# Kernel optimization log

Hardware: AMD Instinct MI355X
Metric: run time of the kernel (lower is better)

The kernel has to match this reference:

```python
import jax, jax.numpy as jnp
import numpy as np

NUM_SLOTS = 8
DIM = 256
ITERS = 3
EPS_LN = 1e-5

def _ln(x, g, b):
    mu = jnp.mean(x, axis=-1, keepdims=True)
    var = jnp.var(x, axis=-1, keepdims=True)
    return (x - mu) * jax.lax.rsqrt(var + EPS_LN) * g + b

def setup_inputs() -> dict:
    key = jax.random.key(0)
    ks = jax.random.split(key, 16)
    d = DIM
    s = 1.0 / np.sqrt(d)
    inp = {
        'x': jax.random.normal(ks[0], (64, 4096, d), jnp.float32),
        'noise': jax.random.normal(ks[1], (64, NUM_SLOTS, d), jnp.float32),
        'slots_mu': jax.random.normal(ks[2], (1, 1, d), jnp.float32),
        'slots_logsigma': jnp.zeros((1, 1, d), jnp.float32),
        'Wq': jax.random.uniform(ks[3], (d, d), jnp.float32, -s, s),
        'Wk': jax.random.uniform(ks[4], (d, d), jnp.float32, -s, s),
        'Wv': jax.random.uniform(ks[5], (d, d), jnp.float32, -s, s),
        'W_ih': jax.random.uniform(ks[6], (3 * d, d), jnp.float32, -s, s),
        'W_hh': jax.random.uniform(ks[7], (3 * d, d), jnp.float32, -s, s),
        'b_ih': jax.random.uniform(ks[8], (3 * d,), jnp.float32, -s, s),
        'b_hh': jax.random.uniform(ks[9], (3 * d,), jnp.float32, -s, s),
        'W1': jax.random.uniform(ks[10], (d, d), jnp.float32, -s, s),
        'b1': jax.random.uniform(ks[11], (d,), jnp.float32, -s, s),
        'W2': jax.random.uniform(ks[12], (d, d), jnp.float32, -s, s),
        'b2': jax.random.uniform(ks[13], (d,), jnp.float32, -s, s),
        'g_in': jnp.ones((d,), jnp.float32), 'be_in': jnp.zeros((d,), jnp.float32),
        'g_sl': jnp.ones((d,), jnp.float32), 'be_sl': jnp.zeros((d,), jnp.float32),
        'g_ff': jnp.ones((d,), jnp.float32), 'be_ff': jnp.zeros((d,), jnp.float32),
    }
    return inp

def _gru(x, h, W_ih, W_hh, b_ih, b_hh):
    # torch.nn.GRUCell math; x,h: [M, d]
    gi = x @ W_ih.T + b_ih
    gh = h @ W_hh.T + b_hh
    i_r, i_z, i_n = jnp.split(gi, 3, axis=-1)
    h_r, h_z, h_n = jnp.split(gh, 3, axis=-1)
    r = jax.nn.sigmoid(i_r + h_r)
    z = jax.nn.sigmoid(i_z + h_z)
    n = jnp.tanh(i_n + r * h_n)
    return (1.0 - z) * n + z * h

def reference(x, noise, slots_mu, slots_logsigma, Wq, Wk, Wv, W_ih, W_hh, b_ih, b_hh,
              W1, b1, W2, b2, g_in, be_in, g_sl, be_sl, g_ff, be_ff):
    B, N, d = x.shape
    scale = d ** (-0.5)
    x = _ln(x, g_in, be_in)
    slots = slots_mu + noise * jnp.exp(slots_logsigma)  # [B, K, d]
    # k/v are loop-invariant; hoist (same math as original)
    k = jnp.einsum('bnd,ed->bne', x, Wk)
    v = jnp.einsum('bnd,ed->bne', x, Wv)
    for _ in range(ITERS):
        slots_prev = slots
        q = jnp.einsum('bkd,ed->bke', _ln(slots, g_sl, be_sl), Wq)
        attn = jax.nn.softmax(jnp.einsum('bkd,bnd->bkn', q, k) * scale, axis=-1) + 1e-8
        attn = attn / jnp.sum(attn, axis=-1, keepdims=True)
        updates = jnp.einsum('bkn,bnd->bkd', attn, v)
        slots = _gru(updates.reshape(-1, d), slots_prev.reshape(-1, d),
                     W_ih, W_hh, b_ih, b_hh).reshape(B, NUM_SLOTS, d)
        h = jax.nn.relu(jnp.einsum('bkd,ed->bke', _ln(slots, g_ff, be_ff), W1) + b1)
        slots = slots + jnp.einsum('bkd,ed->bke', h, W2) + b2
    return slots.reshape(B, NUM_SLOTS * d)
```

## Files before the change

kernel.cpp:

```cpp
#include <hip/hip_runtime.h>
#include <cstddef>

#define DIM 256
#define NSLOT 8
#define BATCH 64
#define NTOK 4096
#define SEGB 16
#define NPART SEGB
#define ITERS 3
#define EPS 1e-5f

typedef short bf16x8 __attribute__((ext_vector_type(8)));
typedef short bf16x4 __attribute__((ext_vector_type(4)));
typedef float f32x4  __attribute__((ext_vector_type(4)));

static __device__ __forceinline__ short f2bf(float f) {
    union { float f; unsigned u; } v; v.f = f;
    unsigned r = v.u + 0x7fffu + ((v.u >> 16) & 1u);
    return (short)(r >> 16);
}

enum : size_t {
    OFF_M     = 0,
    OFF_WIHT  = OFF_M    + 256 * 256,
    OFF_WHHT  = OFF_WIHT + 256 * 768,
    OFF_WVT   = OFF_WHHT + 256 * 768,
    OFF_W1T   = OFF_WVT  + 256 * 256,
    OFF_W2T   = OFF_W1T  + 256 * 256,
    OFF_SLOTS = OFF_W2T  + 256 * 256,
    OFF_SNEW  = OFF_SLOTS + BATCH * NSLOT * 256,
    OFF_QT    = OFF_SNEW  + BATCH * NSLOT * 256,
    OFF_H     = OFF_QT    + BATCH * NSLOT * 256,
    OFF_UPD   = OFF_H     + BATCH * NSLOT * 256,
    OFF_UPART = OFF_UPD   + BATCH * NSLOT * 256,
    OFF_LPART = OFF_UPART + (size_t)BATCH * NPART * NSLOT * 256,
    OFF_XLN   = OFF_LPART + BATCH * NPART * 16,
    WS_FLOATS = OFF_XLN   + (size_t)BATCH * NTOK * 128
};

__global__ __launch_bounds__(256) void k_transpose(const float* __restrict__ w_ih,
                                                   const float* __restrict__ w_hh,
                                                   const float* __restrict__ wv,
                                                   const float* __restrict__ w1,
                                                   const float* __restrict__ w2,
                                                   float* __restrict__ ws) {
    int z = blockIdx.z;
    const float* src;
    float* dst;
    int R;
    if (z == 0)      { src = w_ih; dst = ws + OFF_WIHT; R = 768; }
    else if (z == 1) { src = w_hh; dst = ws + OFF_WHHT; R = 768; }
    else if (z == 2) { src = wv;   dst = ws + OFF_WVT;  R = 256; }
    else if (z == 3) { src = w1;   dst = ws + OFF_W1T;  R = 256; }
    else             { src = w2;   dst = ws + OFF_W2T;  R = 256; }
    if ((int)blockIdx.x * 32 >= R) return;
    __shared__ float tile[32][33];
    int lx = threadIdx.x & 31, ly = threadIdx.x >> 5;
    int r0 = blockIdx.x * 32, c0 = blockIdx.y * 32;
#pragma unroll
    for (int p = 0; p < 4; ++p)
        tile[ly + p * 8][lx] = src[(size_t)(r0 + ly + p * 8) * 256 + c0 + lx];
    __syncthreads();
#pragma unroll
    for (int p = 0; p < 4; ++p)
        dst[(size_t)(c0 + ly + p * 8) * R + r0 + lx] = tile[lx][ly + p * 8];
}

__global__ __launch_bounds__(256) void k_m(const float* __restrict__ wq,
                                           const float* __restrict__ wk,
                                           float* __restrict__ ws) {
    int d = blockIdx.x, t = threadIdx.x;
    float acc = 0.f;
    for (int e = 0; e < 256; ++e)
        acc += wq[e * 256 + d] * wk[e * 256 + t];
    ws[OFF_M + d * 256 + t] = acc * 0.0625f;
}

__global__ __launch_bounds__(256) void k_init(const float* __restrict__ mu,
                                              const float* __restrict__ logsig,
                                              const float* __restrict__ noise,
                                              float* __restrict__ ws) {
    int i = blockIdx.x * 256 + threadIdx.x;
    int d = i & 255;
    ws[OFF_SLOTS + i] = mu[d] + noise[i] * __expf(logsig[d]);
}

__global__ __launch_bounds__(256) void k_qt(float* __restrict__ ws,
                                            const float* __restrict__ g_sl,
                                            const float* __restrict__ be_sl) {
    __shared__ float ln[2048];
    int chunk = blockIdx.x, b = blockIdx.y;
    int t = threadIdx.x, wave = t >> 6, lane = t & 63;
    const float* slots = ws + OFF_SLOTS + b * 2048;
    float4 gf = ((const float4*)g_sl)[lane];
    float4 bf = ((const float4*)be_sl)[lane];
#pragma unroll
    for (int rr = 0; rr < 2; ++rr) {
        int r = wave + rr * 4;
        float4 v = ((const float4*)(slots + r * 256))[lane];
        float s1 = v.x + v.y + v.z + v.w;
        float s2 = v.x * v.x + v.y * v.y + v.z * v.z + v.w * v.w;
#pragma unroll
        for (int m = 1; m < 64; m <<= 1) { s1 += __shfl_xor(s1, m); s2 += __shfl_xor(s2, m); }
        float mu = s1 * (1.f / 256.f);
        float rstd = rsqrtf(s2 * (1.f / 256.f) - mu * mu + EPS);
        float4 o;
        o.x = (v.x - mu) * rstd * gf.x + bf.x;
        o.y = (v.y - mu) * rstd * gf.y + bf.y;
        o.z = (v.z - mu) * rstd * gf.z + bf.z;
        o.w = (v.w - mu) * rstd * gf.w + bf.w;
        *((float4*)&ln[r * 256 + lane * 4]) = o;
    }
    __syncthreads();
    const float* M = ws + OFF_M;
    int k0 = t >> 6;
    int e = chunk * 64 + (t & 63);
    float a0 = 0.f, a1 = 0.f;
    for (int d = 0; d < 256; ++d) {
        float m = M[d * 256 + e];
        a0 += ln[k0 * 256 + d] * m;
        a1 += ln[(k0 + 4) * 256 + d] * m;
    }
    float* qt = ws + OFF_QT + b * 2048;
    qt[k0 * 256 + e] = a0;
    qt[(k0 + 4) * 256 + e] = a1;
}

template <bool P1>
__global__ __launch_bounds__(256) void k_attn_t(const float* __restrict__ x,
                                                const float* __restrict__ g_in,
                                                const float* __restrict__ be_in,
                                                float* __restrict__ ws) {
    int seg = blockIdx.x, b = blockIdx.y;
    int t = threadIdx.x;
    int w = t >> 6, lane = t & 63;
    int q = lane >> 4, s16 = lane & 15;

    __shared__ short qhi[8 * 264];
    __shared__ short xT[256 * 64];
    __shared__ short Etmp[16 * 72];
    __shared__ float lsum[4][8];

    const float* qtg = ws + OFF_QT + b * 2048;
    for (int idx = t; idx < 8 * 264; idx += 256) {
        int s = idx >> 8;
        s = idx / 264;
        int d = idx - s * 264;
        qhi[idx] = (d < 256) ? f2bf(qtg[s * 256 + d]) : (short)0;
    }
    __syncthreads();

    bf16x8 qf[8];
#pragma unroll
    for (int i = 0; i < 8; ++i) {
        if (s16 < 8) qf[i] = *(const bf16x8*)&qhi[s16 * 264 + i * 32 + q * 8];
        else         qf[i] = (bf16x8){0, 0, 0, 0, 0, 0, 0, 0};
    }

    f32x4 U[4];
#pragma unroll
    for (int c = 0; c < 4; ++c) U[c] = (f32x4){0.f, 0.f, 0.f, 0.f};
    float lacc = 0.f;

    short* xln = (short*)(ws + OFF_XLN);
    int mytok = seg * 256 + w * 16 + s16;
    int g0 = ((w * 16 + s16) >> 3);
    int t7 = s16 & 7;

    bf16x8 af[8];
    if (!P1) {
        const short* xr = xln + ((size_t)b * NTOK + mytok) * 256 + q * 8;
#pragma unroll
        for (int i = 0; i < 8; ++i) af[i] = *(const bf16x8*)&xr[i * 32];
    }

    for (int tt = 0; tt < 4; ++tt) {
        int tok = mytok + tt * 64;
        if (P1) {
            const float4* xp = (const float4*)(x + ((size_t)b * NTOK + tok) * 256 + q * 8);
            float4 xa[8], xb[8];
#pragma unroll
            for (int i = 0; i < 8; ++i) { xa[i] = xp[8 * i]; xb[i] = xp[8 * i + 1]; }
            float s1 = 0.f, s2 = 0.f;
#pragma unroll
            for (int i = 0; i < 8; ++i) {
                s1 += xa[i].x + xa[i].y + xa[i].z + xa[i].w + xb[i].x + xb[i].y + xb[i].z + xb[i].w;
                s2 += xa[i].x * xa[i].x + xa[i].y * xa[i].y + xa[i].z * xa[i].z + xa[i].w * xa[i].w
                    + xb[i].x * xb[i].x + xb[i].y * xb[i].y + xb[i].z * xb[i].z + xb[i].w * xb[i].w;
            }
            s1 += __shfl_xor(s1, 16); s2 += __shfl_xor(s2, 16);
            s1 += __shfl_xor(s1, 32); s2 += __shfl_xor(s2, 32);
            float mu = s1 * (1.f / 256.f);
            float rstd = rsqrtf(s2 * (1.f / 256.f) - mu * mu + EPS);
            short* xrow = xln + ((size_t)b * NTOK + tok) * 256;
#pragma unroll
            for (int i = 0; i < 8; ++i) {
                int dbase = i * 32 + q * 8;
                float4 gA = *(const float4*)&g_in[dbase];
                float4 gB = *(const float4*)&g_in[dbase + 4];
                float4 bA = *(const float4*)&be_in[dbase];
                float4 bB = *(const float4*)&be_in[dbase + 4];
                bf16x8 f;
                f[0] = f2bf((xa[i].x - mu) * rstd * gA.x + bA.x);
                f[1] = f2bf((xa[i].y - mu) * rstd * gA.y + bA.y);
                f[2] = f2bf((xa[i].z - mu) * rstd * gA.z + bA.z);
                f[3] = f2bf((xa[i].w - mu) * rstd * gA.w + bA.w);
                f[4] = f2bf((xb[i].x - mu) * rstd * gB.x + bB.x);
                f[5] = f2bf((xb[i].y - mu) * rstd * gB.y + bB.y);
                f[6] = f2bf((xb[i].z - mu) * rstd * gB.z + bB.z);
                f[7] = f2bf((xb[i].w - mu) * rstd * gB.w + bB.w);
                af[i] = f;
                *(bf16x8*)&xrow[i * 32 + q * 8] = f;
            }
        }

        f32x4 Lc0 = (f32x4){0.f, 0.f, 0.f, 0.f};
        f32x4 Lc1 = (f32x4){0.f, 0.f, 0.f, 0.f};
#pragma unroll
        for (int i = 0; i < 4; ++i) {
            Lc0 = __builtin_amdgcn_mfma_f32_16x16x32_bf16(af[i],     qf[i],     Lc0, 0, 0, 0);
            Lc1 = __builtin_amdgcn_mfma_f32_16x16x32_bf16(af[i + 4], qf[i + 4], Lc1, 0, 0, 0);
        }

        bf16x4 e2;
#pragma unroll
        for (int r = 0; r < 4; ++r) {
            float E = __expf(fminf(Lc0[r] + Lc1[r], 30.f));
            lacc += E;
            e2[r] = f2bf(E);
        }

        __syncthreads();

#pragma unroll
        for (int i = 0; i < 8; ++i) {
            int Ki = (4 * i + q) & 7;
            int dbase = i * 32 + q * 8;
            bf16x8 f = af[i];
#pragma unroll
            for (int e = 0; e < 8; ++e) {
                int gp = (g0 ^ e ^ Ki) & 7;
                xT[((dbase + e) << 6) + (gp << 3) + t7] = f[e];
            }
        }
        *(bf16x4*)&Etmp[s16 * 72 + w * 16 + q * 4] = e2;

        __syncthreads();

        bf16x8 afn[8];
        if (!P1 && tt < 3) {
            const short* xr = xln + ((size_t)b * NTOK + tok + 64) * 256 + q * 8;
#pragma unroll
            for (int i = 0; i < 8; ++i) afn[i] = *(const bf16x8*)&xr[i * 32];
        }

        bf16x8 ea0 = *(const bf16x8*)&Etmp[s16 * 72 + q * 8];
        bf16x8 ea1 = *(const bf16x8*)&Etmp[s16 * 72 + 32 + q * 8];
#pragma unroll
        for (int c = 0; c < 4; ++c) {
            int d = (4 * w + c) * 16 + s16;
            int swz = (d ^ (d >> 3)) & 7;
            const short* row = &xT[d << 6];
            bf16x8 b0 = *(const bf16x8*)&row[((q ^ swz) & 7) << 3];
            bf16x8 b1 = *(const bf16x8*)&row[(((4 + q) ^ swz) & 7) << 3];
            U[c] = __builtin_amdgcn_mfma_f32_16x16x32_bf16(ea0, b0, U[c], 0, 0, 0);
            U[c] = __builtin_amdgcn_mfma_f32_16x16x32_bf16(ea1, b1, U[c], 0, 0, 0);
        }

        if (!P1 && tt < 3) {
#pragma unroll
            for (int i = 0; i < 8; ++i) af[i] = afn[i];
        }
    }

    lacc += __shfl_xor(lacc, 16); lacc += __shfl_xor(lacc, 32);
    __syncthreads();
    if (q == 0 && s16 < 8) lsum[w][s16] = lacc;
    __syncthreads();
    float* lpart = ws + OFF_LPART + (size_t)(b * NPART + seg) * 16;
    if (t < 8) lpart[t] = lsum[0][t] + lsum[1][t] + lsum[2][t] + lsum[3][t];
    float* up = ws + OFF_UPART + (size_t)(b * NPART + seg) * NSLOT * 256;
#pragma unroll
    for (int c = 0; c < 4; ++c) {
        int d = (4 * w + c) * 16 + s16;
#pragma unroll
        for (int r = 0; r < 4; ++r) {
            int slot = q * 4 + r;
            if (slot < 8) up[slot * 256 + d] = U[c][r];
        }
    }
}

static __device__ __forceinline__ void ln_row2(const float* src, float* dst,
                                               const float* __restrict__ g,
                                               const float* __restrict__ be,
                                               int wave, int lane) {
    if (wave < 2) {
        float4 v = *(const float4*)(src + wave * 256 + lane * 4);
        float s1 = v.x + v.y + v.z + v.w;
        float s2 = v.x * v.x + v.y * v.y + v.z * v.z + v.w * v.w;
#pragma unroll
        for (int m = 1; m < 64; m <<= 1) { s1 += __shfl_xor(s1, m); s2 += __shfl_xor(s2, m); }
        float mu = s1 * (1.f / 256.f);
        float rstd = rsqrtf(s2 * (1.f / 256.f) - mu * mu + EPS);
        float4 gf = ((const float4*)g)[lane];
        float4 bf = ((const float4*)be)[lane];
        float4 o;
        o.x = (v.x - mu) * rstd * gf.x + bf.x;
        o.y = (v.y - mu) * rstd * gf.y + bf.y;
        o.z = (v.z - mu) * rstd * gf.z + bf.z;
        o.w = (v.w - mu) * rstd * gf.w + bf.w;
        *(float4*)(dst + wave * 256 + lane * 4) = o;
    }
}

__global__ __launch_bounds__(512) void k_fused(float* __restrict__ ws,
                                               const float* __restrict__ b_ih,
                                               const float* __restrict__ b_hh,
                                               const float* __restrict__ g_ff,
                                               const float* __restrict__ be_ff,
                                               const float* __restrict__ b1p,
                                               const float* __restrict__ b2p,
                                               const float* __restrict__ g_sl,
                                               const float* __restrict__ be_sl,
                                               float* __restrict__ dout) {
    __shared__ __align__(16) float uc[2][256], upd[2][256], sl[2][256], snew[2][256];
    __shared__ __align__(16) float lnb[2][256], hbuf[2][256], so[2][256];
    __shared__ float lsv[2];

    int sp = blockIdx.x, b = blockIdx.y, t = threadIdx.x;
    int s0 = sp * 2;
    int s = t >> 8, d = t & 255;
    int wave = t >> 6, lane = t & 63;

    if (t < 32) {
        int ss = t >> 4, g = t & 15;
        float lv = ws[OFF_LPART + (size_t)(b * NPART + g) * 16 + s0 + ss];
#pragma unroll
        for (int m = 1; m < 16; m <<= 1) lv += __shfl_xor(lv, m);
        if ((t & 15) == 0) lsv[ss] = lv;
    }

    const float* up0 = ws + OFF_UPART + (size_t)b * NPART * NSLOT * 256 + (s0 + s) * 256 + d;
    float acc = 0.f;
#pragma unroll
    for (int g = 0; g < NPART; ++g) acc += up0[(size_t)g * NSLOT * 256];
    sl[s][d] = ws[OFF_SLOTS + (size_t)b * 2048 + (s0 + s) * 256 + d];
    __syncthreads();
    uc[s][d] = acc / lsv[s];
    __syncthreads();

    {
        const float* WvT = ws + OFF_WVT;
        float o = 0.f;
        for (int dd = 0; dd < 256; ++dd) o += uc[s][dd] * WvT[dd * 256 + d];
        upd[s][d] = o;
    }
    __syncthreads();

    {
        const float* WihT = ws + OFF_WIHT;
        const float* WhhT = ws + OFF_WHHT;
        float ar = 0.f, az = 0.f, an = 0.f, hr = 0.f, hz = 0.f, hn = 0.f;
        for (int dd = 0; dd < 256; ++dd) {
            float ud = upd[s][dd], sd = sl[s][dd];
            const float* wi = WihT + dd * 768;
            const float* wh = WhhT + dd * 768;
            ar += ud * wi[d];       az += ud * wi[256 + d]; an += ud * wi[512 + d];
            hr += sd * wh[d];       hz += sd * wh[256 + d]; hn += sd * wh[512 + d];
        }
        float rg = 1.f / (1.f + __expf(-(ar + b_ih[d] + hr + b_hh[d])));
        float zg = 1.f / (1.f + __expf(-(az + b_ih[256 + d] + hz + b_hh[256 + d])));
        float ng = tanhf(an + b_ih[512 + d] + rg * (hn + b_hh[512 + d]));
        snew[s][d] = (1.f - zg) * ng + zg * sl[s][d];
    }
    __syncthreads();

    ln_row2(&snew[0][0], &lnb[0][0], g_ff, be_ff, wave, lane);
    __syncthreads();

    {
        const float* W1T = ws + OFF_W1T;
        float o = 0.f;
        for (int dd = 0; dd < 256; ++dd) o += lnb[s][dd] * W1T[dd * 256 + d];
        hbuf[s][d] = fmaxf(o + b1p[d], 0.f);
    }
    __syncthreads();

    {
        const float* W2T = ws + OFF_W2T;
        float o = 0.f;
        for (int dd = 0; dd < 256; ++dd) o += hbuf[s][dd] * W2T[dd * 256 + d];
        float r = snew[s][d] + o + b2p[d];
        so[s][d] = r;
        ws[OFF_SLOTS + (size_t)b * 2048 + (s0 + s) * 256 + d] = r;
        if (dout) dout[(size_t)b * 2048 + (s0 + s) * 256 + d] = r;
    }

    if (!dout) {
        __syncthreads();
        ln_row2(&so[0][0], &lnb[0][0], g_sl, be_sl, wave, lane);
        __syncthreads();
        const float* M = ws + OFF_M;
        float o = 0.f;
        for (int dd = 0; dd < 256; ++dd) o += lnb[s][dd] * M[dd * 256 + d];
        ws[OFF_QT + (size_t)b * 2048 + (s0 + s) * 256 + d] = o;
    }
}

extern "C" void kernel_launch(void* const* d_in, const int* in_sizes, int n_in,
                              void* d_out, int out_size, void* d_ws, size_t ws_size,
                              hipStream_t stream) {
    const float* x      = (const float*)d_in[0];
    const float* noise  = (const float*)d_in[1];
    const float* mu     = (const float*)d_in[2];
    const float* logsig = (const float*)d_in[3];
    const float* Wq     = (const float*)d_in[4];
    const float* Wk     = (const float*)d_in[5];
    const float* Wv     = (const float*)d_in[6];
    const float* W_ih   = (const float*)d_in[7];
    const float* W_hh   = (const float*)d_in[8];
    const float* b_ih   = (const float*)d_in[9];
    const float* b_hh   = (const float*)d_in[10];
    const float* W1     = (const float*)d_in[11];
    const float* b1     = (const float*)d_in[12];
    const float* W2     = (const float*)d_in[13];
    const float* b2     = (const float*)d_in[14];
    const float* g_in   = (const float*)d_in[15];
    const float* be_in  = (const float*)d_in[16];
    const float* g_sl   = (const float*)d_in[17];
    const float* be_sl  = (const float*)d_in[18];
    const float* g_ff   = (const float*)d_in[19];
    const float* be_ff  = (const float*)d_in[20];
    float* ws = (float*)d_ws;
    float* out = (float*)d_out;

    hipLaunchKernelGGL(k_transpose, dim3(24, 8, 5), dim3(256), 0, stream, W_ih, W_hh, Wv, W1, W2, ws);
    hipLaunchKernelGGL(k_m, dim3(256), dim3(256), 0, stream, Wq, Wk, ws);
    hipLaunchKernelGGL(k_init, dim3(512), dim3(256), 0, stream, mu, logsig, noise, ws);
    hipLaunchKernelGGL(k_qt, dim3(4, 64), dim3(256), 0, stream, ws, g_sl, be_sl);
    for (int it = 0; it < ITERS; ++it) {
        if (it == 0)
            hipLaunchKernelGGL((k_attn_t<true>),  dim3(SEGB, 64), dim3(256), 0, stream, x, g_in, be_in, ws);
        else
            hipLaunchKernelGGL((k_attn_t<false>), dim3(SEGB, 64), dim3(256), 0, stream, x, g_in, be_in, ws);
        hipLaunchKernelGGL(k_fused, dim3(4, 64), dim3(512), 0, stream, ws,
                           b_ih, b_hh, g_ff, be_ff, b1, b2, g_sl, be_sl,
                           (it == ITERS - 1) ? out : nullptr);
    }
}
```

Measured before the change: 732.0 us.

## Merge iteration loop into cooperative persistent megakernel with grid syncs

Replaces the per-iteration attention and fused slot-update kernels with one cooperative persistent kernel. Grid-wide syncs separate the phases: attention, update reduction plus the hidden-state GRU GEMM, the input GRU GEMM, the GRU elementwise step, the two MLP GEMMs and the next-iteration q projection. The small GEMMs are split into many 8-row by 64-column tiles so all CUs share the work, replacing the old 256-block kernel that did long serial dot products. This saves launch overhead and spreads the slot MLP/GRU work, at the cost of many grid barriers and possible occupancy loss, with a multi-kernel fallback if the cooperative launch fails.

```diff
diff --git a/kernel.cpp b/kernel.cpp
--- a/kernel.cpp
+++ b/kernel.cpp
@@ -1,5 +1,8 @@
 #include <hip/hip_runtime.h>
+#include <hip/hip_cooperative_groups.h>
 #include <cstddef>
+
+namespace cg = cooperative_groups;
 
 #define DIM 256
 #define NSLOT 8
@@ -35,7 +38,22 @@
     OFF_UPART = OFF_UPD   + BATCH * NSLOT * 256,
     OFF_LPART = OFF_UPART + (size_t)BATCH * NPART * NSLOT * 256,
     OFF_XLN   = OFF_LPART + BATCH * NPART * 16,
-    WS_FLOATS = OFF_XLN   + (size_t)BATCH * NTOK * 128
+    OFF_GH    = OFF_XLN   + (size_t)BATCH * NTOK * 128,
+    OFF_GI    = OFF_GH    + 512 * 768,
+    WS_FLOATS = OFF_GI    + 512 * 768
+};
+
+union MegaShared {
+    struct {
+        short qhi[8 * 264];
+        short xT[256 * 64];
+        short Etmp[16 * 72];
+        float lsum[4][8];
+    } a;
+    struct {
+        float At[8][256];
+        float lrow[8];
+    } g;
 };
 
 __global__ __launch_bounds__(256) void k_transpose(const float* __restrict__ w_ih,
@@ -126,34 +144,28 @@
     qt[(k0 + 4) * 256 + e] = a1;
 }
 
-template <bool P1>
-__global__ __launch_bounds__(256) void k_attn_t(const float* __restrict__ x,
-                                                const float* __restrict__ g_in,
-                                                const float* __restrict__ be_in,
-                                                float* __restrict__ ws) {
-    int seg = blockIdx.x, b = blockIdx.y;
-    int t = threadIdx.x;
+__device__ __forceinline__ void attn_phase(bool p1, int unit, int t,
+                                           const float* __restrict__ x,
+                                           const float* __restrict__ g_in,
+                                           const float* __restrict__ be_in,
+                                           float* __restrict__ ws,
+                                           MegaShared& sh) {
+    int seg = unit & 15, b = unit >> 4;
     int w = t >> 6, lane = t & 63;
     int q = lane >> 4, s16 = lane & 15;
 
-    __shared__ short qhi[8 * 264];
-    __shared__ short xT[256 * 64];
-    __shared__ short Etmp[16 * 72];
-    __shared__ float lsum[4][8];
-
     const float* qtg = ws + OFF_QT + b * 2048;
     for (int idx = t; idx < 8 * 264; idx += 256) {
-        int s = idx >> 8;
-        s = idx / 264;
+        int s = idx / 264;
         int d = idx - s * 264;
-        qhi[idx] = (d < 256) ? f2bf(qtg[s * 256 + d]) : (short)0;
+        sh.a.qhi[idx] = (d < 256) ? f2bf(qtg[s * 256 + d]) : (short)0;
     }
     __syncthreads();
 
     bf16x8 qf[8];
 #pragma unroll
     for (int i = 0; i < 8; ++i) {
-        if (s16 < 8) qf[i] = *(const bf16x8*)&qhi[s16 * 264 + i * 32 + q * 8];
+        if (s16 < 8) qf[i] = *(const bf16x8*)&sh.a.qhi[s16 * 264 + i * 32 + q * 8];
         else         qf[i] = (bf16x8){0, 0, 0, 0, 0, 0, 0, 0};
     }
 
@@ -168,7 +180,7 @@
     int t7 = s16 & 7;
 
     bf16x8 af[8];
-    if (!P1) {
+    if (!p1) {
         const short* xr = xln + ((size_t)b * NTOK + mytok) * 256 + q * 8;
 #pragma unroll
         for (int i = 0; i < 8; ++i) af[i] = *(const bf16x8*)&xr[i * 32];
@@ -176,17 +188,15 @@
 
     for (int tt = 0; tt < 4; ++tt) {
         int tok = mytok + tt * 64;
-        if (P1) {
+        if (p1) {
             const float4* xp = (const float4*)(x + ((size_t)b * NTOK + tok) * 256 + q * 8);
-            float4 xa[8], xb[8];
-#pragma unroll
-            for (int i = 0; i < 8; ++i) { xa[i] = xp[8 * i]; xb[i] = xp[8 * i + 1]; }
             float s1 = 0.f, s2 = 0.f;
 #pragma unroll
             for (int i = 0; i < 8; ++i) {
-                s1 += xa[i].x + xa[i].y + xa[i].z + xa[i].w + xb[i].x + xb[i].y + xb[i].z + xb[i].w;
-                s2 += xa[i].x * xa[i].x + xa[i].y * xa[i].y + xa[i].z * xa[i].z + xa[i].w * xa[i].w
-                    + xb[i].x * xb[i].x + xb[i].y * xb[i].y + xb[i].z * xb[i].z + xb[i].w * xb[i].w;
+                float4 a = xp[8 * i], bv = xp[8 * i + 1];
+                s1 += a.x + a.y + a.z + a.w + bv.x + bv.y + bv.z + bv.w;
+                s2 += a.x * a.x + a.y * a.y + a.z * a.z + a.w * a.w
+                    + bv.x * bv.x + bv.y * bv.y + bv.z * bv.z + bv.w * bv.w;
             }
             s1 += __shfl_xor(s1, 16); s2 += __shfl_xor(s2, 16);
             s1 += __shfl_xor(s1, 32); s2 += __shfl_xor(s2, 32);
@@ -195,22 +205,23 @@
             short* xrow = xln + ((size_t)b * NTOK + tok) * 256;
 #pragma unroll
             for (int i = 0; i < 8; ++i) {
+                float4 a = xp[8 * i], bv = xp[8 * i + 1];
                 int dbase = i * 32 + q * 8;
                 float4 gA = *(const float4*)&g_in[dbase];
                 float4 gB = *(const float4*)&g_in[dbase + 4];
                 float4 bA = *(const float4*)&be_in[dbase];
                 float4 bB = *(const float4*)&be_in[dbase + 4];
                 bf16x8 f;
-                f[0] = f2bf((xa[i].x - mu) * rstd * gA.x + bA.x);
-                f[1] = f2bf((xa[i].y - mu) * rstd * gA.y + bA.y);
-                f[2] = f2bf((xa[i].z - mu) * rstd * gA.z + bA.z);
-                f[3] = f2bf((xa[i].w - mu) * rstd * gA.w + bA.w);
-                f[4] = f2bf((xb[i].x - mu) * rstd * gB.x + bB.x);
-                f[5] = f2bf((xb[i].y - mu) * rstd * gB.y + bB.y);
-                f[6] = f2bf((xb[i].z - mu) * rstd * gB.z + bB.z);
-                f[7] = f2bf((xb[i].w - mu) * rstd * gB.w + bB.w);
+                f[0] = f2bf((a.x - mu) * rstd * gA.x + bA.x);
+                f[1] = f2bf((a.y - mu) * rstd * gA.y + bA.y);
+                f[2] = f2bf((a.z - mu) * rstd * gA.z + bA.z);
+                f[3] = f2bf((a.w - mu) * rstd * gA.w + bA.w);
+                f[4] = f2bf((bv.x - mu) * rstd * gB.x + bB.x);
+                f[5] = f2bf((bv.y - mu) * rstd * gB.y + bB.y);
+                f[6] = f2bf((bv.z - mu) * rstd * gB.z + bB.z);
+                f[7] = f2bf((bv.w - mu) * rstd * gB.w + bB.w);
                 af[i] = f;
-                *(bf16x8*)&xrow[i * 32 + q * 8] = f;
+                *(bf16x8*)&xrow[dbase] = f;
             }
         }
 
@@ -240,45 +251,39 @@
 #pragma unroll
             for (int e = 0; e < 8; ++e) {
                 int gp = (g0 ^ e ^ Ki) & 7;
-                xT[((dbase + e) << 6) + (gp << 3) + t7] = f[e];
+                sh.a.xT[((dbase + e) << 6) + (gp << 3) + t7] = f[e];
             }
         }
-        *(bf16x4*)&Etmp[s16 * 72 + w * 16 + q * 4] = e2;
+        *(bf16x4*)&sh.a.Etmp[s16 * 72 + w * 16 + q * 4] = e2;
 
         __syncthreads();
 
-        bf16x8 afn[8];
-        if (!P1 && tt < 3) {
+        if (!p1 && tt < 3) {
             const short* xr = xln + ((size_t)b * NTOK + tok + 64) * 256 + q * 8;
 #pragma unroll
-            for (int i = 0; i < 8; ++i) afn[i] = *(const bf16x8*)&xr[i * 32];
-        }
-
-        bf16x8 ea0 = *(const bf16x8*)&Etmp[s16 * 72 + q * 8];
-        bf16x8 ea1 = *(const bf16x8*)&Etmp[s16 * 72 + 32 + q * 8];
+            for (int i = 0; i < 8; ++i) af[i] = *(const bf16x8*)&xr[i * 32];
+        }
+
+        bf16x8 ea0 = *(const bf16x8*)&sh.a.Etmp[s16 * 72 + q * 8];
+        bf16x8 ea1 = *(const bf16x8*)&sh.a.Etmp[s16 * 72 + 32 + q * 8];
 #pragma unroll
         for (int c = 0; c < 4; ++c) {
             int d = (4 * w + c) * 16 + s16;
             int swz = (d ^ (d >> 3)) & 7;
-            const short* row = &xT[d << 6];
+            const short* row = &sh.a.xT[d << 6];
             bf16x8 b0 = *(const bf16x8*)&row[((q ^ swz) & 7) << 3];
             bf16x8 b1 = *(const bf16x8*)&row[(((4 + q) ^ swz) & 7) << 3];
             U[c] = __builtin_amdgcn_mfma_f32_16x16x32_bf16(ea0, b0, U[c], 0, 0, 0);
             U[c] = __builtin_amdgcn_mfma_f32_16x16x32_bf16(ea1, b1, U[c], 0, 0, 0);
         }
-
-        if (!P1 && tt < 3) {
-#pragma unroll
-            for (int i = 0; i < 8; ++i) af[i] = afn[i];
-        }
     }
 
     lacc += __shfl_xor(lacc, 16); lacc += __shfl_xor(lacc, 32);
     __syncthreads();
-    if (q == 0 && s16 < 8) lsum[w][s16] = lacc;
+    if (q == 0 && s16 < 8) sh.a.lsum[w][s16] = lacc;
     __syncthreads();
     float* lpart = ws + OFF_LPART + (size_t)(b * NPART + seg) * 16;
-    if (t < 8) lpart[t] = lsum[0][t] + lsum[1][t] + lsum[2][t] + lsum[3][t];
+    if (t < 8) lpart[t] = sh.a.lsum[0][t] + sh.a.lsum[1][t] + sh.a.lsum[2][t] + sh.a.lsum[3][t];
     float* up = ws + OFF_UPART + (size_t)(b * NPART + seg) * NSLOT * 256;
 #pragma unroll
     for (int c = 0; c < 4; ++c) {
@@ -291,121 +296,253 @@
     }
 }
 
-static __device__ __forceinline__ void ln_row2(const float* src, float* dst,
-                                               const float* __restrict__ g,
-                                               const float* __restrict__ be,
-                                               int wave, int lane) {
-    if (wave < 2) {
-        float4 v = *(const float4*)(src + wave * 256 + lane * 4);
-        float s1 = v.x + v.y + v.z + v.w;
-        float s2 = v.x * v.x + v.y * v.y + v.z * v.z + v.w * v.w;
-#pragma unroll
-        for (int m = 1; m < 64; m <<= 1) { s1 += __shfl_xor(s1, m); s2 += __shfl_xor(s2, m); }
-        float mu = s1 * (1.f / 256.f);
-        float rstd = rsqrtf(s2 * (1.f / 256.f) - mu * mu + EPS);
+enum { GF_LN = 1, GF_RELU = 2, GF_BIAS = 4, GF_ADD = 8, GF_OUT = 16 };
+
+template <int C, int FLAGS>
+__device__ __forceinline__ void gemm_full(MegaShared& sh, int t,
+        const float* __restrict__ A, const float* __restrict__ W,
+        float* __restrict__ O, int rtile, int ctile,
+        const float* __restrict__ g, const float* __restrict__ be,
+        const float* __restrict__ bias, const float* __restrict__ addsrc,
+        float* __restrict__ dout) {
+    const int r0 = rtile * 8, c0 = ctile * 64;
+    {
+        int r = t >> 5, c8 = (t & 31) * 8;
+        const float* src = A + (size_t)(r0 + r) * 256 + c8;
+        *(float4*)&sh.g.At[r][c8]     = *(const float4*)src;
+        *(float4*)&sh.g.At[r][c8 + 4] = *(const float4*)(src + 4);
+    }
+    __syncthreads();
+    if (FLAGS & GF_LN) {
+        int wv = t >> 6, lane = t & 63;
         float4 gf = ((const float4*)g)[lane];
         float4 bf = ((const float4*)be)[lane];
-        float4 o;
-        o.x = (v.x - mu) * rstd * gf.x + bf.x;
-        o.y = (v.y - mu) * rstd * gf.y + bf.y;
-        o.z = (v.z - mu) * rstd * gf.z + bf.z;
-        o.w = (v.w - mu) * rstd * gf.w + bf.w;
-        *(float4*)(dst + wave * 256 + lane * 4) = o;
-    }
-}
-
-__global__ __launch_bounds__(512) void k_fused(float* __restrict__ ws,
-                                               const float* __restrict__ b_ih,
-                                               const float* __restrict__ b_hh,
-                                               const float* __restrict__ g_ff,
-                                               const float* __restrict__ be_ff,
-                                               const float* __restrict__ b1p,
-                                               const float* __restrict__ b2p,
-                                               const float* __restrict__ g_sl,
-                                               const float* __restrict__ be_sl,
-                                               float* __restrict__ dout) {
-    __shared__ __align__(16) float uc[2][256], upd[2][256], sl[2][256], snew[2][256];
-    __shared__ __align__(16) float lnb[2][256], hbuf[2][256], so[2][256];
-    __shared__ float lsv[2];
-
-    int sp = blockIdx.x, b = blockIdx.y, t = threadIdx.x;
-    int s0 = sp * 2;
-    int s = t >> 8, d = t & 255;
-    int wave = t >> 6, lane = t & 63;
-
-    if (t < 32) {
-        int ss = t >> 4, g = t & 15;
-        float lv = ws[OFF_LPART + (size_t)(b * NPART + g) * 16 + s0 + ss];
-#pragma unroll
-        for (int m = 1; m < 16; m <<= 1) lv += __shfl_xor(lv, m);
-        if ((t & 15) == 0) lsv[ss] = lv;
-    }
-
-    const float* up0 = ws + OFF_UPART + (size_t)b * NPART * NSLOT * 256 + (s0 + s) * 256 + d;
-    float acc = 0.f;
-#pragma unroll
-    for (int g = 0; g < NPART; ++g) acc += up0[(size_t)g * NSLOT * 256];
-    sl[s][d] = ws[OFF_SLOTS + (size_t)b * 2048 + (s0 + s) * 256 + d];
+#pragma unroll
+        for (int rr = 0; rr < 2; ++rr) {
+            int row = wv + rr * 4;
+            float4 v = *(float4*)&sh.g.At[row][lane * 4];
+            float s1 = v.x + v.y + v.z + v.w;
+            float s2 = v.x * v.x + v.y * v.y + v.z * v.z + v.w * v.w;
+#pragma unroll
+            for (int m = 1; m < 64; m <<= 1) { s1 += __shfl_xor(s1, m); s2 += __shfl_xor(s2, m); }
+            float mu = s1 * (1.f / 256.f);
+            float rstd = rsqrtf(s2 * (1.f / 256.f) - mu * mu + EPS);
+            float4 o;
+            o.x = (v.x - mu) * rstd * gf.x + bf.x;
+            o.y = (v.y - mu) * rstd * gf.y + bf.y;
+            o.z = (v.z - mu) * rstd * gf.z + bf.z;
+            o.w = (v.w - mu) * rstd * gf.w + bf.w;
+            *(float4*)&sh.g.At[row][lane * 4] = o;
+        }
+        __syncthreads();
+    }
+    int ct = t & 63, rt = t >> 6;
+    int c = c0 + ct;
+    float acc0 = 0.f, acc1 = 0.f;
+#pragma unroll 4
+    for (int dd = 0; dd < 256; dd += 4) {
+        float w0 = W[(size_t)(dd + 0) * C + c];
+        float w1 = W[(size_t)(dd + 1) * C + c];
+        float w2 = W[(size_t)(dd + 2) * C + c];
+        float w3 = W[(size_t)(dd + 3) * C + c];
+        float4 a0 = *(const float4*)&sh.g.At[rt * 2 + 0][dd];
+        float4 a1 = *(const float4*)&sh.g.At[rt * 2 + 1][dd];
+        acc0 += a0.x * w0 + a0.y * w1 + a0.z * w2 + a0.w * w3;
+        acc1 += a1.x * w0 + a1.y * w1 + a1.z * w2 + a1.w * w3;
+    }
+    float bb = (FLAGS & GF_BIAS) ? bias[c] : 0.f;
+    int r = r0 + rt * 2;
+    float v0 = acc0 + bb, v1 = acc1 + bb;
+    if (FLAGS & GF_RELU) { v0 = fmaxf(v0, 0.f); v1 = fmaxf(v1, 0.f); }
+    if (FLAGS & GF_ADD)  { v0 += addsrc[(size_t)r * 256 + c]; v1 += addsrc[(size_t)(r + 1) * 256 + c]; }
+    O[(size_t)r * C + c] = v0;
+    O[(size_t)(r + 1) * C + c] = v1;
+    if (FLAGS & GF_OUT) {
+        if (dout) { dout[(size_t)r * 256 + c] = v0; dout[(size_t)(r + 1) * 256 + c] = v1; }
+    }
+}
+
+__device__ __forceinline__ void phase_upd(MegaShared& sh, int t, float* __restrict__ ws,
+                                          int rtile, int ctile) {
+    const int r0 = rtile * 8, c0 = ctile * 64;
+    if (t < 8) {
+        int rr = r0 + t, b = rr >> 3, s = rr & 7;
+        float l = 0.f;
+#pragma unroll
+        for (int g = 0; g < NPART; ++g)
+            l += ws[OFF_LPART + (size_t)(b * NPART + g) * 16 + s];
+        sh.g.lrow[t] = l;
+    }
+    {
+        int r = t >> 5, c8 = (t & 31) * 8;
+        int rr = r0 + r, b = rr >> 3, s = rr & 7;
+        const float* base = ws + OFF_UPART + (size_t)b * (NPART * 2048) + (size_t)s * 256 + c8;
+        float a0 = 0.f, a1 = 0.f, a2 = 0.f, a3 = 0.f, a4 = 0.f, a5 = 0.f, a6 = 0.f, a7 = 0.f;
+#pragma unroll
+        for (int g = 0; g < NPART; ++g) {
+            const float4* p = (const float4*)(base + (size_t)g * 2048);
+            float4 u0 = p[0], u1 = p[1];
+            a0 += u0.x; a1 += u0.y; a2 += u0.z; a3 += u0.w;
+            a4 += u1.x; a5 += u1.y; a6 += u1.z; a7 += u1.w;
+        }
+        __syncthreads();
+        float inv = 1.f / sh.g.lrow[r];
+        float4 o0 = {a0 * inv, a1 * inv, a2 * inv, a3 * inv};
+        float4 o1 = {a4 * inv, a5 * inv, a6 * inv, a7 * inv};
+        *(float4*)&sh.g.At[r][c8]     = o0;
+        *(float4*)&sh.g.At[r][c8 + 4] = o1;
+    }
     __syncthreads();
-    uc[s][d] = acc / lsv[s];
-    __syncthreads();
-
-    {
-        const float* WvT = ws + OFF_WVT;
-        float o = 0.f;
-        for (int dd = 0; dd < 256; ++dd) o += uc[s][dd] * WvT[dd * 256 + d];
-        upd[s][d] = o;
-    }
-    __syncthreads();
-
-    {
-        const float* WihT = ws + OFF_WIHT;
-        const float* WhhT = ws + OFF_WHHT;
-        float ar = 0.f, az = 0.f, an = 0.f, hr = 0.f, hz = 0.f, hn = 0.f;
-        for (int dd = 0; dd < 256; ++dd) {
-            float ud = upd[s][dd], sd = sl[s][dd];
-            const float* wi = WihT + dd * 768;
-            const float* wh = WhhT + dd * 768;
-            ar += ud * wi[d];       az += ud * wi[256 + d]; an += ud * wi[512 + d];
-            hr += sd * wh[d];       hz += sd * wh[256 + d]; hn += sd * wh[512 + d];
-        }
-        float rg = 1.f / (1.f + __expf(-(ar + b_ih[d] + hr + b_hh[d])));
-        float zg = 1.f / (1.f + __expf(-(az + b_ih[256 + d] + hz + b_hh[256 + d])));
-        float ng = tanhf(an + b_ih[512 + d] + rg * (hn + b_hh[512 + d]));
-        snew[s][d] = (1.f - zg) * ng + zg * sl[s][d];
-    }
-    __syncthreads();
-
-    ln_row2(&snew[0][0], &lnb[0][0], g_ff, be_ff, wave, lane);
-    __syncthreads();
-
-    {
-        const float* W1T = ws + OFF_W1T;
-        float o = 0.f;
-        for (int dd = 0; dd < 256; ++dd) o += lnb[s][dd] * W1T[dd * 256 + d];
-        hbuf[s][d] = fmaxf(o + b1p[d], 0.f);
-    }
-    __syncthreads();
-
-    {
-        const float* W2T = ws + OFF_W2T;
-        float o = 0.f;
-        for (int dd = 0; dd < 256; ++dd) o += hbuf[s][dd] * W2T[dd * 256 + d];
-        float r = snew[s][d] + o + b2p[d];
-        so[s][d] = r;
-        ws[OFF_SLOTS + (size_t)b * 2048 + (s0 + s) * 256 + d] = r;
-        if (dout) dout[(size_t)b * 2048 + (s0 + s) * 256 + d] = r;
-    }
-
-    if (!dout) {
-        __syncthreads();
-        ln_row2(&so[0][0], &lnb[0][0], g_sl, be_sl, wave, lane);
-        __syncthreads();
-        const float* M = ws + OFF_M;
-        float o = 0.f;
-        for (int dd = 0; dd < 256; ++dd) o += lnb[s][dd] * M[dd * 256 + d];
-        ws[OFF_QT + (size_t)b * 2048 + (s0 + s) * 256 + d] = o;
-    }
+    int ct = t & 63, rt = t >> 6;
+    int c = c0 + ct;
+    const float* W = ws + OFF_WVT;
+    float acc0 = 0.f, acc1 = 0.f;
+#pragma unroll 4
+    for (int dd = 0; dd < 256; dd += 4) {
+        float w0 = W[(size_t)(dd + 0) * 256 + c];
+        float w1 = W[(size_t)(dd + 1) * 256 + c];
+        float w2 = W[(size_t)(dd + 2) * 256 + c];
+        float w3 = W[(size_t)(dd + 3) * 256 + c];
+        float4 a0 = *(const float4*)&sh.g.At[rt * 2 + 0][dd];
+        float4 a1 = *(const float4*)&sh.g.At[rt * 2 + 1][dd];
+        acc0 += a0.x * w0 + a0.y * w1 + a0.z * w2 + a0.w * w3;
+        acc1 += a1.x * w0 + a1.y * w1 + a1.z * w2 + a1.w * w3;
+    }
+    float* O = ws + OFF_UPD;
+    int r = r0 + rt * 2;
+    O[(size_t)r * 256 + c] = acc0;
+    O[(size_t)(r + 1) * 256 + c] = acc1;
+}
+
+__device__ __forceinline__ void phase_gru(int u, int t, float* __restrict__ ws,
+                                          const float* __restrict__ b_ih,
+                                          const float* __restrict__ b_hh) {
+    int idx = u * 256 + t;
+    int c = idx & 255;
+    size_t r = (size_t)(idx >> 8);
+    const float* GI = ws + OFF_GI;
+    const float* GH = ws + OFF_GH;
+    float gir = GI[r * 768 + c], giz = GI[r * 768 + 256 + c], gin2 = GI[r * 768 + 512 + c];
+    float ghr = GH[r * 768 + c], ghz = GH[r * 768 + 256 + c], ghn = GH[r * 768 + 512 + c];
+    float hv = ws[OFF_SLOTS + idx];
+    float rg = 1.f / (1.f + __expf(-(gir + b_ih[c] + ghr + b_hh[c])));
+    float zg = 1.f / (1.f + __expf(-(giz + b_ih[256 + c] + ghz + b_hh[256 + c])));
+    float ng = tanhf(gin2 + b_ih[512 + c] + rg * (ghn + b_hh[512 + c]));
+    ws[OFF_SNEW + idx] = (1.f - zg) * ng + zg * hv;
+}
+
+__global__ __launch_bounds__(256, 4) void k_mega(
+        const float* __restrict__ x,
+        const float* __restrict__ g_in, const float* __restrict__ be_in,
+        const float* __restrict__ b_ih, const float* __restrict__ b_hh,
+        const float* __restrict__ g_ff, const float* __restrict__ be_ff,
+        const float* __restrict__ b1p, const float* __restrict__ b2p,
+        const float* __restrict__ g_sl, const float* __restrict__ be_sl,
+        float* __restrict__ ws, float* __restrict__ dout) {
+    cg::grid_group gg = cg::this_grid();
+    __shared__ MegaShared sh;
+    int t = threadIdx.x;
+    int G = gridDim.x;
+
+    for (int it = 0; it < ITERS; ++it) {
+        bool p1 = (it == 0), last = (it == ITERS - 1);
+        for (int u = blockIdx.x; u < 1024; u += G) {
+            attn_phase(p1, u, t, x, g_in, be_in, ws, sh);
+            __syncthreads();
+        }
+        gg.sync();
+        for (int u = blockIdx.x; u < 1024; u += G) {
+            if (u < 256) phase_upd(sh, t, ws, u >> 2, u & 3);
+            else {
+                int k = u - 256;
+                gemm_full<768, 0>(sh, t, ws + OFF_SLOTS, ws + OFF_WHHT, ws + OFF_GH,
+                                  k / 12, k % 12, nullptr, nullptr, nullptr, nullptr, nullptr);
+            }
+            __syncthreads();
+        }
+        gg.sync();
+        for (int u = blockIdx.x; u < 768; u += G) {
+            gemm_full<768, 0>(sh, t, ws + OFF_UPD, ws + OFF_WIHT, ws + OFF_GI,
+                              u / 12, u % 12, nullptr, nullptr, nullptr, nullptr, nullptr);
+            __syncthreads();
+        }
+        gg.sync();
+        for (int u = blockIdx.x; u < 512; u += G)
+            phase_gru(u, t, ws, b_ih, b_hh);
+        gg.sync();
+        for (int u = blockIdx.x; u < 256; u += G) {
+            gemm_full<256, GF_LN | GF_BIAS | GF_RELU>(sh, t, ws + OFF_SNEW, ws + OFF_W1T,
+                              ws + OFF_H, u >> 2, u & 3, g_ff, be_ff, b1p, nullptr, nullptr);
+            __syncthreads();
+        }
+        gg.sync();
+        for (int u = blockIdx.x; u < 256; u += G) {
+            gemm_full<256, GF_BIAS | GF_ADD | GF_OUT>(sh, t, ws + OFF_H, ws + OFF_W2T,
+                              ws + OFF_SLOTS, u >> 2, u & 3, nullptr, nullptr, b2p,
+                              ws + OFF_SNEW, last ? dout : nullptr);
+            __syncthreads();
+        }
+        gg.sync();
+        if (!last) {
+            for (int u = blockIdx.x; u < 256; u += G) {
+                gemm_full<256, GF_LN>(sh, t, ws + OFF_SLOTS, ws + OFF_M, ws + OFF_QT,
+                                      u >> 2, u & 3, g_sl, be_sl, nullptr, nullptr, nullptr);
+                __syncthreads();
+            }
+            gg.sync();
+        }
+    }
+}
+
+__global__ __launch_bounds__(256) void k_attn_fb(const float* __restrict__ x,
+                                                 const float* __restrict__ g_in,
+                                                 const float* __restrict__ be_in,
+                                                 float* __restrict__ ws, int p1) {
+    __shared__ MegaShared sh;
+    attn_phase(p1 != 0, blockIdx.x, threadIdx.x, x, g_in, be_in, ws, sh);
+}
+__global__ __launch_bounds__(256) void k_phB_fb(float* __restrict__ ws) {
+    __shared__ MegaShared sh;
+    int u = blockIdx.x, t = threadIdx.x;
+    if (u < 256) phase_upd(sh, t, ws, u >> 2, u & 3);
+    else {
+        int k = u - 256;
+        gemm_full<768, 0>(sh, t, ws + OFF_SLOTS, ws + OFF_WHHT, ws + OFF_GH,
+                          k / 12, k % 12, nullptr, nullptr, nullptr, nullptr, nullptr);
+    }
+}
+__global__ __launch_bounds__(256) void k_phC_fb(float* __restrict__ ws) {
+    __shared__ MegaShared sh;
+    gemm_full<768, 0>(sh, threadIdx.x, ws + OFF_UPD, ws + OFF_WIHT, ws + OFF_GI,
+                      blockIdx.x / 12, blockIdx.x % 12, nullptr, nullptr, nullptr, nullptr, nullptr);
+}
+__global__ __launch_bounds__(256) void k_phD_fb(float* __restrict__ ws,
+                                                const float* __restrict__ b_ih,
+                                                const float* __restrict__ b_hh) {
+    phase_gru(blockIdx.x, threadIdx.x, ws, b_ih, b_hh);
+}
+__global__ __launch_bounds__(256) void k_phF1_fb(float* __restrict__ ws,
+                                                 const float* __restrict__ g_ff,
+                                                 const float* __restrict__ be_ff,
+                                                 const float* __restrict__ b1p) {
+    __shared__ MegaShared sh;
+    gemm_full<256, GF_LN | GF_BIAS | GF_RELU>(sh, threadIdx.x, ws + OFF_SNEW, ws + OFF_W1T,
+                      ws + OFF_H, blockIdx.x >> 2, blockIdx.x & 3, g_ff, be_ff, b1p, nullptr, nullptr);
+}
+__global__ __launch_bounds__(256) void k_phF2_fb(float* __restrict__ ws,
+                                                 const float* __restrict__ b2p,
+                                                 float* __restrict__ dout) {
+    __shared__ MegaShared sh;
+    gemm_full<256, GF_BIAS | GF_ADD | GF_OUT>(sh, threadIdx.x, ws + OFF_H, ws + OFF_W2T,
+                      ws + OFF_SLOTS, blockIdx.x >> 2, blockIdx.x & 3, nullptr, nullptr, b2p,
+                      ws + OFF_SNEW, dout);
+}
+__global__ __launch_bounds__(256) void k_phG_fb(float* __restrict__ ws,
+                                                const float* __restrict__ g_sl,
+                                                const float* __restrict__ be_sl) {
+    __shared__ MegaShared sh;
+    gemm_full<256, GF_LN>(sh, threadIdx.x, ws + OFF_SLOTS, ws + OFF_M, ws + OFF_QT,
+                          blockIdx.x >> 2, blockIdx.x & 3, g_sl, be_sl, nullptr, nullptr, nullptr);
 }
 
 extern "C" void kernel_launch(void* const* d_in, const int* in_sizes, int n_in,
@@ -439,13 +576,51 @@
     hipLaunchKernelGGL(k_m, dim3(256), dim3(256), 0, stream, Wq, Wk, ws);
     hipLaunchKernelGGL(k_init, dim3(512), dim3(256), 0, stream, mu, logsig, noise, ws);
     hipLaunchKernelGGL(k_qt, dim3(4, 64), dim3(256), 0, stream, ws, g_sl, be_sl);
-    for (int it = 0; it < ITERS; ++it) {
-        if (it == 0)
-            hipLaunchKernelGGL((k_attn_t<true>),  dim3(SEGB, 64), dim3(256), 0, stream, x, g_in, be_in, ws);
-        else
-            hipLaunchKernelGGL((k_attn_t<false>), dim3(SEGB, 64), dim3(256), 0, stream, x, g_in, be_in, ws);
-        hipLaunchKernelGGL(k_fused, dim3(4, 64), dim3(512), 0, stream, ws,
-                           b_ih, b_hh, g_ff, be_ff, b1, b2, g_sl, be_sl,
-                           (it == ITERS - 1) ? out : nullptr);
-    }
-}
+
+    int perCU = 0;
+    hipError_t qerr = hipOccupancyMaxActiveBlocksPerMultiprocessor(&perCU, k_mega, 256, 0);
+    int grid = 0;
+    if (qerr == hipSuccess && perCU > 0) {
+        long cap = (long)perCU * 256;
+        if (cap >= 1024)      grid = 1024;
+        else if (cap >= 512)  grid = 512;
+        else if (cap >= 256)  grid = 256;
+    }
+
+    bool launched = false;
+    if (grid > 0) {
+        void* args[13];
+        args[0]  = (void*)&x;
+        args[1]  = (void*)&g_in;
+        args[2]  = (void*)&be_in;
+        args[3]  = (void*)&b_ih;
+        args[4]  = (void*)&b_hh;
+        args[5]  = (void*)&g_ff;
+        args[6]  = (void*)&be_ff;
+        args[7]  = (void*)&b1;
+        args[8]  = (void*)&b2;
+        args[9]  = (void*)&g_sl;
+        args[10] = (void*)&be_sl;
+        args[11] = (void*)&ws;
+        args[12] = (void*)&out;
+        hipError_t lerr = hipLaunchCooperativeKernel((const void*)k_mega, dim3(grid), dim3(256),
+                                                     args, 0, stream);
+        launched = (lerr == hipSuccess);
+    }
+
+    if (!launched) {
+        for (int it = 0; it < ITERS; ++it) {
+            bool last = (it == ITERS - 1);
+            hipLaunchKernelGGL(k_attn_fb, dim3(1024), dim3(256), 0, stream, x, g_in, be_in, ws,
+                               (it == 0) ? 1 : 0);
+            hipLaunchKernelGGL(k_phB_fb, dim3(1024), dim3(256), 0, stream, ws);
+            hipLaunchKernelGGL(k_phC_fb, dim3(768), dim3(256), 0, stream, ws);
+            hipLaunchKernelGGL(k_phD_fb, dim3(512), dim3(256), 0, stream, ws, b_ih, b_hh);
+            hipLaunchKernelGGL(k_phF1_fb, dim3(256), dim3(256), 0, stream, ws, g_ff, be_ff, b1);
+            hipLaunchKernelGGL(k_phF2_fb, dim3(256), dim3(256), 0, stream, ws, b2,
+                               last ? out : nullptr);
+            if (!last)
+                hipLaunchKernelGGL(k_phG_fb, dim3(256), dim3(256), 0, stream, ws, g_sl, be_sl);
+        }
+    }
+}
```

New measurement: 2.354 ms. 3.22x slower.
